# Kernel optimization log

Measured on AMD Instinct MI355X. Metric: run time of the kernel, lower is better.

Reference implementation:

```python
import jax, jax.numpy as jnp
import numpy as np

ALPHA = 2.0
INF = jnp.float32(1e30)
EPS = jnp.float32(1e-12)


def _pairwise_d2(h, w):
    # Squared Euclidean distance between all pixel pairs of an h x w grid. [N, N]
    yy, xx = jnp.meshgrid(jnp.arange(h), jnp.arange(w), indexing='ij')
    pts = jnp.stack([yy.reshape(-1), xx.reshape(-1)], axis=-1).astype(jnp.float32)  # [N, 2]
    diff = pts[:, None, :] - pts[None, :, :]
    return jnp.sum(diff * diff, axis=-1)


def _edt(mask, d2):
    # scipy.distance_transform_edt semantics: for each pixel, Euclidean distance
    # to the nearest zero (False) pixel. mask: [N] bool, d2: [N, N].
    m = jnp.min(jnp.where(mask[None, :], INF, d2), axis=1)
    return jnp.where(jnp.any(~mask), jnp.sqrt(m), 0.0)


def _distance_field(img, d2):
    # Faithful port of HausdorffDTLoss.distance_field for one 2D image.
    h, w = img.shape
    fg = (img > 0.5).reshape(-1)
    fgd = _edt(fg, d2)            # edt(fg_mask)
    bgd = _edt(~fg, d2)           # edt(bg_mask)
    fg_any = jnp.any(fg)
    bg_any = jnp.any(~fg)
    fmax = jnp.maximum(jnp.max(fgd), EPS)
    bmax = jnp.maximum(jnp.max(bgd), EPS)
    field = (jnp.where(fg_any, fgd / fmax, 0.0)
             + jnp.where(fg_any & bg_any, bgd / bmax, 0.0))
    return field.reshape(h, w)


def setup_inputs() -> dict:
    key = jax.random.key(0)
    k1, k2, k3 = jax.random.split(key, 3)
    R, C, H, W = 128, 80, 28, 28
    preds = jax.random.normal(k1, (R, C, H, W), dtype=jnp.float32)
    targets = jax.random.uniform(k2, (R, H, W), dtype=jnp.float32)
    labels = jax.random.randint(k3, (R,), 0, C)
    return {"preds": preds, "targets": targets, "labels": labels}


def reference(preds, targets, labels):
    R, C, H, W = preds.shape
    d2 = _pairwise_d2(H, W)
    p = jax.nn.sigmoid(preds)
    # pred = preds[i][labels[i]]  -> gather the per-ROI class channel
    p_sel = jnp.take_along_axis(p, labels[:, None, None, None], axis=1)[:, 0]  # [R, H, W]
    df = lambda im: _distance_field(im, d2)
    preds_dt = jax.vmap(df)(p_sel)      # [R, H, W]
    targets_dt = jax.vmap(df)(targets)  # [R, H, W]
    dist = preds_dt ** ALPHA + targets_dt ** ALPHA
    # torch loop accumulates `distance` across samples without resetting -> cumsum
    cum = jnp.cumsum(dist, axis=0)
    err = (p_sel - targets) ** 2
    hd_loss = jnp.sum(jnp.mean(err * cum, axis=(1, 2))) / R
    return hd_loss
```

## Files before the change

### kernel.cpp

```cpp
#include <hip/hip_runtime.h>

#define R 128
#define C 80
#define HH 28
#define WW 28
#define NPIX 784
#define BIGD (1 << 26)

__global__ __launch_bounds__(256) void edt_field_kernel(
    const float* __restrict__ preds,
    const float* __restrict__ targets,
    const int* __restrict__ labels,
    float* __restrict__ distP_t,
    float* __restrict__ distT_t,
    float* __restrict__ err_t,
    float* __restrict__ out)
{
    __shared__ unsigned fgrow[HH];
    __shared__ int rowd[2][HH][WW];
    __shared__ int md2[NPIX];
    __shared__ int redF[256], redB[256];
    __shared__ float invF, invB;
    __shared__ int s_uniform;

    const int tid = threadIdx.x;
    const int b = blockIdx.x;

    if (b == 0 && tid == 0) out[0] = 0.0f;

    if (tid < HH) fgrow[tid] = 0u;
    __syncthreads();

    const bool isPred = (b < R);
    const int rb = isPred ? b : (b - R);
    const float* src;
    const float* tgt = targets + (size_t)rb * NPIX;
    if (isPred) {
        const int lab = labels[b];
        src = preds + ((size_t)b * C + (size_t)lab) * NPIX;
    } else {
        src = tgt;
    }

    for (int j = tid; j < NPIX; j += 256) {
        float v = src[j];
        float s;
        if (isPred) {
            s = 1.0f / (1.0f + expf(-v));
            const float e = s - tgt[j];
            err_t[(size_t)j * R + b] = e * e;
        } else {
            s = v;
        }
        if (s > 0.5f) {
            atomicOr(&fgrow[j / WW], 1u << (j % WW));
        }
    }
    __syncthreads();

    for (int e = tid; e < 2 * NPIX; e += 256) {
        const int c = (e >= NPIX);
        const int rem = e - c * NPIX;
        const int r = rem / WW;
        const int x = rem - r * WW;
        const unsigned fr = fgrow[r];
        const unsigned w = c ? fr : (~fr & 0x0FFFFFFFu);
        int dv;
        if (w == 0u) {
            dv = BIGD;
        } else {
            const unsigned wl = w & ((2u << x) - 1u);
            const unsigned wr = w >> x;
            const int dl = wl ? (x - (31 - __builtin_clz(wl))) : 10000;
            const int dr = wr ? __builtin_ctz(wr) : 10000;
            const int d = dl < dr ? dl : dr;
            dv = d * d;
        }
        rowd[c][r][x] = dv;
    }
    __syncthreads();

    int localF = -1, localB = -1;
    for (int j = tid; j < NPIX; j += 256) {
        const int y = j / WW;
        const int x = j - y * WW;
        const int c = (fgrow[y] >> x) & 1;
        const int* rd = &rowd[c ^ 1][0][x];
        int m = 0x3FFFFFFF;
        #pragma unroll
        for (int r = 0; r < HH; ++r) {
            const int dy = y - r;
            const int cand = dy * dy + rd[r * WW];
            m = cand < m ? cand : m;
        }
        md2[j] = m;
        if (c) localF = m > localF ? m : localF;
        else   localB = m > localB ? m : localB;
    }
    redF[tid] = localF;
    redB[tid] = localB;
    __syncthreads();
    for (int s = 128; s > 0; s >>= 1) {
        if (tid < s) {
            redF[tid] = redF[tid + s] > redF[tid] ? redF[tid + s] : redF[tid];
            redB[tid] = redB[tid + s] > redB[tid] ? redB[tid + s] : redB[tid];
        }
        __syncthreads();
    }
    if (tid == 0) {
        const int mF = redF[0], mB = redB[0];
        if (mF < 0 || mB < 0) {
            s_uniform = 1; invF = 0.0f; invB = 0.0f;
        } else {
            s_uniform = 0;
            invF = 1.0f / (float)mF;
            invB = 1.0f / (float)mB;
        }
    }
    __syncthreads();

    float* dst = isPred ? distP_t : distT_t;
    const int uni = s_uniform;
    for (int j = tid; j < NPIX; j += 256) {
        float fsq = 0.0f;
        if (!uni) {
            const int y = j / WW;
            const int x = j - y * WW;
            const int c = (fgrow[y] >> x) & 1;
            fsq = (float)md2[j] * (c ? invF : invB);
        }
        dst[(size_t)j * R + rb] = fsq;
    }
}

__global__ __launch_bounds__(128) void scan_reduce_kernel(
    const float* __restrict__ distP_t,
    const float* __restrict__ distT_t,
    const float* __restrict__ err_t,
    float* __restrict__ out)
{
    __shared__ float wsum;
    __shared__ float bacc[2];

    const int px = blockIdx.x;
    const int i = threadIdx.x;
    const size_t o = (size_t)px * R + i;

    float cum = distP_t[o] + distT_t[o];
    const float e2 = err_t[o];

    #pragma unroll
    for (int off = 1; off < 64; off <<= 1) {
        const float v = __shfl_up(cum, off, 64);
        if ((i & 63) >= off) cum += v;
    }
    if (i == 63) wsum = cum;
    __syncthreads();
    if (i >= 64) cum += wsum;

    float acc = e2 * cum;
    #pragma unroll
    for (int off = 32; off > 0; off >>= 1)
        acc += __shfl_down(acc, off, 64);
    if ((i & 63) == 0) bacc[i >> 6] = acc;
    __syncthreads();
    if (i == 0)
        atomicAdd(out, (bacc[0] + bacc[1]) * (1.0f / ((float)R * (float)NPIX)));
}

extern "C" void kernel_launch(void* const* d_in, const int* in_sizes, int n_in,
                              void* d_out, int out_size, void* d_ws, size_t ws_size,
                              hipStream_t stream) {
    const float* preds = (const float*)d_in[0];
    const float* targets = (const float*)d_in[1];
    const int* labels = (const int*)d_in[2];
    float* out = (float*)d_out;

    float* ws = (float*)d_ws;
    float* distP_t = ws;
    float* distT_t = ws + (size_t)R * NPIX;
    float* err_t   = ws + (size_t)2 * R * NPIX;

    hipLaunchKernelGGL(edt_field_kernel, dim3(2 * R), dim3(256), 0, stream,
                       preds, targets, labels, distP_t, distT_t, err_t, out);
    hipLaunchKernelGGL(scan_reduce_kernel, dim3(NPIX), dim3(128), 0, stream,
                       distP_t, distT_t, err_t, out);
}
```

Baseline: 91.84 us.

## Fuse EDT and scan-reduce into one cooperative kernel with grid sync

Merges the two kernels into a single cooperative launch that uses a grid-wide barrier between the distance-field phase and the cumulative-sum reduction phase. The second phase now assigns one wavefront per pixel, with each lane handling two ROIs loaded as float2, so each wave scans all 128 ROIs without shared-memory combining. The aim is to remove the second launch and its inter-kernel gap. In exchange it adds grid-sync overhead and requires all 256 blocks to be co-resident. The out[0]=0 write by block 0 is still ordered before the atomics by the grid sync.

```diff
diff --git a/kernel.cpp b/kernel.cpp
--- a/kernel.cpp
+++ b/kernel.cpp
@@ -1,4 +1,7 @@
 #include <hip/hip_runtime.h>
+#include <hip/hip_cooperative_groups.h>
+
+namespace cg = cooperative_groups;
 
 #define R 128
 #define C 80
@@ -7,7 +10,7 @@
 #define NPIX 784
 #define BIGD (1 << 26)
 
-__global__ __launch_bounds__(256) void edt_field_kernel(
+__global__ __launch_bounds__(256) void hd_loss_coop(
     const float* __restrict__ preds,
     const float* __restrict__ targets,
     const int* __restrict__ labels,
@@ -131,41 +134,35 @@
         }
         dst[(size_t)j * R + rb] = fsq;
     }
-}
 
-__global__ __launch_bounds__(128) void scan_reduce_kernel(
-    const float* __restrict__ distP_t,
-    const float* __restrict__ distT_t,
-    const float* __restrict__ err_t,
-    float* __restrict__ out)
-{
-    __shared__ float wsum;
-    __shared__ float bacc[2];
+    __threadfence();
+    cg::grid_group grid = cg::this_grid();
+    grid.sync();
 
-    const int px = blockIdx.x;
-    const int i = threadIdx.x;
-    const size_t o = (size_t)px * R + i;
-
-    float cum = distP_t[o] + distT_t[o];
-    const float e2 = err_t[o];
-
-    #pragma unroll
-    for (int off = 1; off < 64; off <<= 1) {
-        const float v = __shfl_up(cum, off, 64);
-        if ((i & 63) >= off) cum += v;
+    const int wv = (b << 2) + (tid >> 6);
+    const int lane = tid & 63;
+    if (wv < NPIX) {
+        const size_t o = (size_t)wv * R + 2 * lane;
+        const float2 dp = *(const float2*)(distP_t + o);
+        const float2 dt = *(const float2*)(distT_t + o);
+        const float2 e2 = *(const float2*)(err_t + o);
+        const float d0 = dp.x + dt.x;
+        const float d1 = dp.y + dt.y;
+        float s = d0 + d1;
+        #pragma unroll
+        for (int off = 1; off < 64; off <<= 1) {
+            const float v = __shfl_up(s, off, 64);
+            if (lane >= off) s += v;
+        }
+        const float cum1 = s;
+        const float cum0 = s - d1;
+        float acc = e2.x * cum0 + e2.y * cum1;
+        #pragma unroll
+        for (int off = 32; off > 0; off >>= 1)
+            acc += __shfl_down(acc, off, 64);
+        if (lane == 0)
+            atomicAdd(out, acc * (1.0f / ((float)R * (float)NPIX)));
     }
-    if (i == 63) wsum = cum;
-    __syncthreads();
-    if (i >= 64) cum += wsum;
-
-    float acc = e2 * cum;
-    #pragma unroll
-    for (int off = 32; off > 0; off >>= 1)
-        acc += __shfl_down(acc, off, 64);
-    if ((i & 63) == 0) bacc[i >> 6] = acc;
-    __syncthreads();
-    if (i == 0)
-        atomicAdd(out, (bacc[0] + bacc[1]) * (1.0f / ((float)R * (float)NPIX)));
 }
 
 extern "C" void kernel_launch(void* const* d_in, const int* in_sizes, int n_in,
@@ -181,8 +178,8 @@
     float* distT_t = ws + (size_t)R * NPIX;
     float* err_t   = ws + (size_t)2 * R * NPIX;
 
-    hipLaunchKernelGGL(edt_field_kernel, dim3(2 * R), dim3(256), 0, stream,
-                       preds, targets, labels, distP_t, distT_t, err_t, out);
-    hipLaunchKernelGGL(scan_reduce_kernel, dim3(NPIX), dim3(128), 0, stream,
-                       distP_t, distT_t, err_t, out);
+    void* args[] = {(void*)&preds, (void*)&targets, (void*)&labels,
+                    (void*)&distP_t, (void*)&distT_t, (void*)&err_t, (void*)&out};
+    hipLaunchCooperativeKernel((void*)hd_loss_coop, dim3(2 * R), dim3(256),
+                               args, 0, stream);
 }
```

After: 159.0 us. 73.1% more time.
